# Kernel tuning notes

Hardware: AMD Instinct MI355X
Metric: run time of the kernel (lower is better)

## Reference

```python
import jax, jax.numpy as jnp
import numpy as np

S, B, I, H, O = 1024, 64, 512, 2048, 512


def setup_inputs() -> dict:
    key = jax.random.key(0)
    k1, k2, k3, k4, k5 = jax.random.split(key, 5)
    X = jax.random.normal(k1, (S, B, I), dtype=jnp.float32)
    W_ih = jax.random.normal(k2, (H, I), dtype=jnp.float32) * (1.0 / np.sqrt(I))
    hh = jax.random.uniform(k3, (H,), dtype=jnp.float32)  # clamped-to-[-1,1] diagonal recurrence
    W_ho = jax.random.normal(k4, (O, H), dtype=jnp.float32) * (1.0 / np.sqrt(H))
    b_ho = jax.random.normal(k5, (O,), dtype=jnp.float32) * 0.01
    return {"X": X, "W_ih": W_ih, "hh": hh, "W_ho": W_ho, "b_ho": b_ho}


def reference(X, W_ih, hh, W_ho, b_ho):
    # Batch the input->hidden projection over the whole sequence in one GEMM:
    # u[s,b,h] = X[s,b,i] @ W_ih[h,i]^T
    u = jnp.einsum('sbi,hi->sbh', X, W_ih)
    h0 = jnp.zeros((X.shape[1], W_ih.shape[0]), dtype=X.dtype)

    def step(h, u_t):
        h_new = jnp.abs(u_t + hh * h)
        return h_new, None

    h_final, _ = jax.lax.scan(step, h0, u)
    Y = h_final @ W_ho.T + b_ho  # [B, O]
    return Y
```

## Files before the change

kernel.cpp:

```cpp
#include <hip/hip_runtime.h>
#include <hip/hip_bf16.h>
#include <stdint.h>

#define S_LEN 1024
#define B_SZ  64
#define I_SZ  512
#define H_SZ  2048
#define O_SZ  512

typedef __bf16  bf16x8 __attribute__((ext_vector_type(8)));
typedef float   f32x4  __attribute__((ext_vector_type(4)));

static __device__ __forceinline__ ushort f2bf(float f) {
  union { float f; unsigned u; } v; v.f = f;
  unsigned r = v.u + 0x7FFFu + ((v.u >> 16) & 1u);
  return (ushort)(r >> 16);
}
static __device__ __forceinline__ float bf2f(ushort u) {
  return __builtin_bit_cast(float, (unsigned)u << 16);
}

#define GLOAD_LDS16(gp, lp) \
  __builtin_amdgcn_global_load_lds( \
      (__attribute__((address_space(1))) void*)(gp), \
      (__attribute__((address_space(3))) void*)(lp), 16, 0, 0)

__global__ __launch_bounds__(256) void convert_f32_bf16_kernel(
    const float4* __restrict__ in, ushort4* __restrict__ out, int n4) {
  int i = blockIdx.x * 256 + threadIdx.x;
  if (i >= n4) return;
  float4 v = in[i];
  ushort4 o; o.x = f2bf(v.x); o.y = f2bf(v.y); o.z = f2bf(v.z); o.w = f2bf(v.w);
  out[i] = o;
}

__global__ __launch_bounds__(256) void convert_x_kernel(
    const float* __restrict__ X, ushort* __restrict__ Xt) {
  const int row  = blockIdx.x * 4 + (threadIdx.x >> 6);
  const int lane = threadIdx.x & 63;
  const int s = row >> 6, b = row & 63;
  const float* src = X + (size_t)row * I_SZ + lane * 8;
  float4 v0 = *(const float4*)src;
  float4 v1 = *(const float4*)(src + 4);
  union { ushort h[8]; uint4 v; } o;
  o.h[0] = f2bf(v0.x); o.h[1] = f2bf(v0.y); o.h[2] = f2bf(v0.z); o.h[3] = f2bf(v0.w);
  o.h[4] = f2bf(v1.x); o.h[5] = f2bf(v1.y); o.h[6] = f2bf(v1.z); o.h[7] = f2bf(v1.w);
  *(uint4*)(Xt + ((size_t)b * S_LEN + s) * I_SZ + lane * 8) = o.v;
}

__global__ __launch_bounds__(256) void init_y_kernel(
    const float* __restrict__ bho, float* __restrict__ Y) {
  int idx = blockIdx.x * 256 + threadIdx.x;
  Y[idx] = bho[idx & (O_SZ - 1)];
}

#define SCAN16(colp, s0_) do { \
    ushort4 v0 = *(const ushort4*)&(colp)[(s0_)]; \
    ushort4 v1 = *(const ushort4*)&(colp)[(s0_) + 4]; \
    ushort4 v2 = *(const ushort4*)&(colp)[(s0_) + 8]; \
    ushort4 v3 = *(const ushort4*)&(colp)[(s0_) + 12]; \
    p = fmaf(c, fabsf(p), bf2f(v0.x)); p = fmaf(c, fabsf(p), bf2f(v0.y)); \
    p = fmaf(c, fabsf(p), bf2f(v0.z)); p = fmaf(c, fabsf(p), bf2f(v0.w)); \
    p = fmaf(c, fabsf(p), bf2f(v1.x)); p = fmaf(c, fabsf(p), bf2f(v1.y)); \
    p = fmaf(c, fabsf(p), bf2f(v1.z)); p = fmaf(c, fabsf(p), bf2f(v1.w)); \
    p = fmaf(c, fabsf(p), bf2f(v2.x)); p = fmaf(c, fabsf(p), bf2f(v2.y)); \
    p = fmaf(c, fabsf(p), bf2f(v2.z)); p = fmaf(c, fabsf(p), bf2f(v2.w)); \
    p = fmaf(c, fabsf(p), bf2f(v3.x)); p = fmaf(c, fabsf(p), bf2f(v3.y)); \
    p = fmaf(c, fabsf(p), bf2f(v3.z)); p = fmaf(c, fabsf(p), bf2f(v3.w)); \
  } while (0)

#define STAGE(dA, dB, T) do { \
    const ushort* ga_ = gA + (size_t)((T) >> 4) * (128 * I_SZ) + ((T) & 15) * 32; \
    const ushort* gb_ = gB + ((T) & 15) * 32; \
    GLOAD_LDS16(ga_,              (dA) + stOff); \
    GLOAD_LDS16(ga_ + 16 * I_SZ,  (dA) + stOff + 512); \
    GLOAD_LDS16(gb_,              (dB) + stOff); \
    GLOAD_LDS16(gb_ + 16 * I_SZ,  (dB) + stOff + 512); \
  } while (0)

__global__ __launch_bounds__(256) void fused_gemm_scan_kernel(
    const ushort* __restrict__ Xbf,
    const ushort* __restrict__ Wbf,
    const float* __restrict__ hh,
    const float* __restrict__ Who,
    float* __restrict__ Y) {
  __shared__ __align__(16) ushort smem[33024];
  ushort* Cs = smem + 16384;

  const int tid  = threadIdx.x;
  const int wave = tid >> 6;
  const int lane = tid & 63;

  const int bid = blockIdx.x;
  const int xcd = bid & 7;
  const int g   = bid >> 3;
  const int b   = (xcd << 3) | (g & 7);
  const int ht  = g >> 3;

  const int wm = (wave >> 1) * 64;
  const int wn = (wave & 1) * 64;
  const int ml = lane & 15;
  const int q  = lane >> 4;

  const int r0     = wave * 32;
  const int lrow   = lane >> 2;
  const int lchunk = ((lane & 3) - lrow) & 3;
  const ushort* gA = Xbf + (size_t)b * (S_LEN * I_SZ)
                   + (size_t)(r0 + lrow) * I_SZ + lchunk * 8;
  const ushort* gB = Wbf + (size_t)(ht * 128 + r0 + lrow) * I_SZ + lchunk * 8;
  const int stOff = r0 * 32;

  const int foff = ((q + ml) & 3) * 8;
  int arow[4], brow[4];
  #pragma unroll
  for (int i = 0; i < 4; ++i) {
    arow[i] = (wm + i * 16 + ml) * 32;
    brow[i] = (wn + i * 16 + ml) * 32;
  }

  float c = 0.0f, p = 0.0f;
  if (tid < 128) c = hh[ht * 128 + tid];

  ushort* curA = smem;          ushort* curB = smem + 4096;
  ushort* nxtA = smem + 8192;   ushort* nxtB = smem + 12288;

  STAGE(curA, curB, 0);
  __syncthreads();

  f32x4 acc[4][4];

  #pragma unroll 1
  for (int t = 0; t < 128; ++t) {
    if ((t & 15) == 0) {
      #pragma unroll
      for (int mi = 0; mi < 4; ++mi)
        #pragma unroll
        for (int ni = 0; ni < 4; ++ni) {
          f32x4 z = {0.f, 0.f, 0.f, 0.f};
          acc[mi][ni] = z;
        }
    }

    if (t < 127) STAGE(nxtA, nxtB, t + 1);

    {
      bf16x8 af[4], bfr[4];
      #pragma unroll
      for (int i = 0; i < 4; ++i) {
        af[i]  = *(const bf16x8*)&curA[arow[i] + foff];
        bfr[i] = *(const bf16x8*)&curB[brow[i] + foff];
      }
      __builtin_amdgcn_s_setprio(1);
      #pragma unroll
      for (int mi = 0; mi < 4; ++mi)
        #pragma unroll
        for (int ni = 0; ni < 4; ++ni)
          acc[mi][ni] = __builtin_amdgcn_mfma_f32_16x16x32_bf16(
              af[mi], bfr[ni], acc[mi][ni], 0, 0, 0);
      __builtin_amdgcn_s_setprio(0);
    }

    if ((t & 15) == 15) {
      const int sb = wm + q * 4;
      #pragma unroll
      for (int mi = 0; mi < 4; ++mi) {
        #pragma unroll
        for (int ni = 0; ni < 4; ++ni) {
          ushort4 o;
          o.x = f2bf(acc[mi][ni][0]); o.y = f2bf(acc[mi][ni][1]);
          o.z = f2bf(acc[mi][ni][2]); o.w = f2bf(acc[mi][ni][3]);
          *(ushort4*)&Cs[(wn + ni * 16 + ml) * 130 + sb + mi * 16] = o;
        }
      }
    }

    __syncthreads();

    if ((t & 15) == 15 && tid < 128) {
      const ushort* col = &Cs[tid * 130];
      #pragma unroll
      for (int s0 = 0; s0 < 128; s0 += 16) {
        SCAN16(col, s0);
      }
    }

    ushort* tA = curA; curA = nxtA; nxtA = tA;
    ushort* tB = curB; curB = nxtB; nxtB = tB;
  }

  if (tid < 128) ((float*)smem)[tid] = fabsf(p);
  __syncthreads();

  {
    const float* hs = (const float*)smem;
    const float* w0 = Who + (size_t)tid * H_SZ + (size_t)ht * 128;
    const float* w1 = w0 + (size_t)256 * H_SZ;
    float y0 = 0.f, y1 = 0.f;
    #pragma unroll 8
    for (int k = 0; k < 128; k += 4) {
      float4 hv = *(const float4*)&hs[k];
      float4 u0 = *(const float4*)&w0[k];
      float4 u1 = *(const float4*)&w1[k];
      y0 += hv.x * u0.x + hv.y * u0.y + hv.z * u0.z + hv.w * u0.w;
      y1 += hv.x * u1.x + hv.y * u1.y + hv.z * u1.z + hv.w * u1.w;
    }
    atomicAdd(&Y[(size_t)b * O_SZ + tid], y0);
    atomicAdd(&Y[(size_t)b * O_SZ + 256 + tid], y1);
  }
}

extern "C" void kernel_launch(void* const* d_in, const int* in_sizes, int n_in,
                              void* d_out, int out_size, void* d_ws, size_t ws_size,
                              hipStream_t stream) {
  (void)in_sizes; (void)n_in; (void)out_size; (void)ws_size;
  const float* X   = (const float*)d_in[0];
  const float* Wih = (const float*)d_in[1];
  const float* hh  = (const float*)d_in[2];
  const float* Who = (const float*)d_in[3];
  const float* bho = (const float*)d_in[4];
  float* Y = (float*)d_out;

  const size_t WBF = (size_t)H_SZ * I_SZ * 2;
  char* w = (char*)d_ws;
  ushort* Wbf = (ushort*)w;
  ushort* Xbf = (ushort*)(w + WBF);

  {
    int n4w = (int)((size_t)H_SZ * I_SZ / 4);
    convert_f32_bf16_kernel<<<n4w / 256, 256, 0, stream>>>(
        (const float4*)Wih, (ushort4*)Wbf, n4w);
  }

  convert_x_kernel<<<(S_LEN * B_SZ) / 4, 256, 0, stream>>>(X, Xbf);

  init_y_kernel<<<(B_SZ * O_SZ) / 256, 256, 0, stream>>>(bho, Y);

  fused_gemm_scan_kernel<<<1024, 256, 0, stream>>>(Xbf, Wbf, hh, Who, Y);
}
```

Baseline: 476.8 us.

## Halve scan staging LDS buffer and change swizzle pattern for bank conflicts

The C tile staging buffer is split into two halves: waves 0-1 write first, the scan consumes 64 rows, then waves 2-3 write and the scan continues. This cuts LDS from about 66KB to about 50KB per block, which may allow more resident blocks per CU. The XOR swizzle for the global-to-LDS staging and the fragment reads is also changed to a pair-granular pattern to alter bank conflicts. In exchange the epilogue needs extra barriers and runs the scan in two serialized phases.

After: 474.4 us. No clear change (-0.5%).

```diff
diff --git a/kernel.cpp b/kernel.cpp
--- a/kernel.cpp
+++ b/kernel.cpp
@@ -84,7 +84,7 @@
     const float* __restrict__ hh,
     const float* __restrict__ Who,
     float* __restrict__ Y) {
-  __shared__ __align__(16) ushort smem[33024];
+  __shared__ __align__(16) ushort smem[24832];
   ushort* Cs = smem + 16384;
 
   const int tid  = threadIdx.x;
@@ -104,13 +104,13 @@
 
   const int r0     = wave * 32;
   const int lrow   = lane >> 2;
-  const int lchunk = ((lane & 3) - lrow) & 3;
+  const int lchunk = ((lane & 3) - (lane >> 3)) & 3;
   const ushort* gA = Xbf + (size_t)b * (S_LEN * I_SZ)
                    + (size_t)(r0 + lrow) * I_SZ + lchunk * 8;
   const ushort* gB = Wbf + (size_t)(ht * 128 + r0 + lrow) * I_SZ + lchunk * 8;
   const int stOff = r0 * 32;
 
-  const int foff = ((q + ml) & 3) * 8;
+  const int foff = ((q + (ml >> 1)) & 3) * 8;
   int arow[4], brow[4];
   #pragma unroll
   for (int i = 0; i < 4; ++i) {
@@ -160,27 +160,41 @@
       __builtin_amdgcn_s_setprio(0);
     }
 
+    __syncthreads();
+
     if ((t & 15) == 15) {
-      const int sb = wm + q * 4;
-      #pragma unroll
-      for (int mi = 0; mi < 4; ++mi) {
-        #pragma unroll
-        for (int ni = 0; ni < 4; ++ni) {
-          ushort4 o;
-          o.x = f2bf(acc[mi][ni][0]); o.y = f2bf(acc[mi][ni][1]);
-          o.z = f2bf(acc[mi][ni][2]); o.w = f2bf(acc[mi][ni][3]);
-          *(ushort4*)&Cs[(wn + ni * 16 + ml) * 130 + sb + mi * 16] = o;
-        }
-      }
-    }
-
-    __syncthreads();
-
-    if ((t & 15) == 15 && tid < 128) {
-      const ushort* col = &Cs[tid * 130];
-      #pragma unroll
-      for (int s0 = 0; s0 < 128; s0 += 16) {
-        SCAN16(col, s0);
+      if (wave < 2) {
+        #pragma unroll
+        for (int mi = 0; mi < 4; ++mi)
+          #pragma unroll
+          for (int ni = 0; ni < 4; ++ni) {
+            ushort4 o;
+            o.x = f2bf(acc[mi][ni][0]); o.y = f2bf(acc[mi][ni][1]);
+            o.z = f2bf(acc[mi][ni][2]); o.w = f2bf(acc[mi][ni][3]);
+            *(ushort4*)&Cs[(wn + ni * 16 + ml) * 66 + mi * 16 + q * 4] = o;
+          }
+      }
+      __syncthreads();
+      if (tid < 128) {
+        const ushort* col = &Cs[tid * 66];
+        SCAN16(col, 0); SCAN16(col, 16); SCAN16(col, 32); SCAN16(col, 48);
+      }
+      __syncthreads();
+      if (wave >= 2) {
+        #pragma unroll
+        for (int mi = 0; mi < 4; ++mi)
+          #pragma unroll
+          for (int ni = 0; ni < 4; ++ni) {
+            ushort4 o;
+            o.x = f2bf(acc[mi][ni][0]); o.y = f2bf(acc[mi][ni][1]);
+            o.z = f2bf(acc[mi][ni][2]); o.w = f2bf(acc[mi][ni][3]);
+            *(ushort4*)&Cs[(wn + ni * 16 + ml) * 66 + mi * 16 + q * 4] = o;
+          }
+      }
+      __syncthreads();
+      if (tid < 128) {
+        const ushort* col = &Cs[tid * 66];
+        SCAN16(col, 0); SCAN16(col, 16); SCAN16(col, 32); SCAN16(col, 48);
       }
     }
 
```
